# Optimization experiments

Hardware: AMD Instinct MI355X
Metric: run time of the kernel (lower is better)

## Reference

```python
import jax, jax.numpy as jnp
import numpy as np

WINDOW = 11
K1, K2, L, EPS = 0.01, 0.03, 1.0, 1e-8


def _box_filter(x, window):
    # Depthwise normalized box filter, VALID padding. x: (B, C, H, W)
    c = x.shape[1]
    k = jnp.ones((c, 1, window, window), dtype=x.dtype) / (window * window)
    return jax.lax.conv_general_dilated(
        x, k, window_strides=(1, 1), padding='VALID',
        dimension_numbers=('NCHW', 'OIHW', 'NCHW'),
        feature_group_count=c)


def setup_inputs() -> dict:
    key = jax.random.key(0)
    kx, ky = jax.random.split(key)
    shape = (16, 3, 512, 512)
    x = jax.random.uniform(kx, shape, dtype=jnp.float32)
    y = jax.random.uniform(ky, shape, dtype=jnp.float32)
    return {"x": x, "y": y}


def reference(x, y):
    C1 = (K1 * L) ** 2
    C2 = (K2 * L) ** 2
    mu_x = _box_filter(x, WINDOW)
    mu_y = _box_filter(y, WINDOW)
    mu_x_sq = mu_x * mu_x
    mu_y_sq = mu_y * mu_y
    mu_xy = mu_x * mu_y
    sigma_x_sq = jnp.maximum(_box_filter(x * x, WINDOW) - mu_x_sq, 0.0)
    sigma_y_sq = jnp.maximum(_box_filter(y * y, WINDOW) - mu_y_sq, 0.0)
    sigma_xy = _box_filter(x * y, WINDOW) - mu_xy
    num = (2.0 * mu_xy + C1) * (2.0 * sigma_xy + C2)
    den = (mu_x_sq + mu_y_sq + C1) * (sigma_x_sq + sigma_y_sq + C2) + EPS
    ssim = jnp.mean(num / den)
    return 1.0 - ssim
```

## Files before the change

### kernel.cpp

```cpp
#include <hip/hip_runtime.h>


#define WIN     11
#define IMG     512
#define OUTW    502
#define SEG     32
#define NSEG    16
#define NPLANES 48
#define RINGN   12
#define STRIDE  516

#define C1f     (0.01f * 0.01f)
#define C2f     (0.03f * 0.03f)
#define EPSf    1e-8f
#define INV121  (1.0f / 121.0f)

__global__ __launch_bounds__(128) void ssim_init(double* acc) {
    acc[0] = 0.0;
}

__global__ __launch_bounds__(128) void ssim_main(const float* __restrict__ x,
                                                 const float* __restrict__ y,
                                                 double* __restrict__ acc) {
    __shared__ float ring[2][RINGN][STRIDE];
    __shared__ float wsum[2];

    const int t     = threadIdx.x;
    const int plane = blockIdx.y;
    const int seg   = blockIdx.x;
    const int o0    = seg * SEG;
    const int o1    = (o0 + SEG < OUTW) ? (o0 + SEG) : OUTW;
    const int r0    = o0;
    const int r1    = o1 + WIN - 2;

    const float* xp = x + (size_t)plane * IMG * IMG;
    const float* yp = y + (size_t)plane * IMG * IMG;

    const int  c0     = 4 * t;
    const bool active = (c0 < OUTW);

    float Vx[14], Vy[14], Vxx[14], Vyy[14], Vxy[14];
#pragma unroll
    for (int j = 0; j < 14; ++j) { Vx[j]=0.f; Vy[j]=0.f; Vxx[j]=0.f; Vyy[j]=0.f; Vxy[j]=0.f; }

    float lsum = 0.0f;

    float4 px = ((const float4*)(xp + (size_t)r0 * IMG))[t];
    float4 py = ((const float4*)(yp + (size_t)r0 * IMG))[t];

    int slot = 0;
    for (int r = r0; r <= r1; ++r) {
        ((float4*)&ring[0][slot][0])[t] = px;
        ((float4*)&ring[1][slot][0])[t] = py;
        if (t < 4) { ring[0][slot][512 + t] = 0.0f; ring[1][slot][512 + t] = 0.0f; }
        if (r < r1) {
            px = ((const float4*)(xp + (size_t)(r + 1) * IMG))[t];
            py = ((const float4*)(yp + (size_t)(r + 1) * IMG))[t];
        }
        __syncthreads();

        if (active) {
            if (r - r0 >= WIN) {
                int os = slot - WIN; if (os < 0) os += RINGN;
                const float4* xr = (const float4*)&ring[0][os][0];
                const float4* yr = (const float4*)&ring[1][os][0];
                float4 a0 = xr[t], a1 = xr[t+1], a2 = xr[t+2], a3 = xr[t+3];
                float4 b0 = yr[t], b1 = yr[t+1], b2 = yr[t+2], b3 = yr[t+3];
                float xn[16], yn[16];
                xn[0]=a0.x; xn[1]=a0.y; xn[2]=a0.z; xn[3]=a0.w;
                xn[4]=a1.x; xn[5]=a1.y; xn[6]=a1.z; xn[7]=a1.w;
                xn[8]=a2.x; xn[9]=a2.y; xn[10]=a2.z; xn[11]=a2.w;
                xn[12]=a3.x; xn[13]=a3.y; xn[14]=a3.z; xn[15]=a3.w;
                yn[0]=b0.x; yn[1]=b0.y; yn[2]=b0.z; yn[3]=b0.w;
                yn[4]=b1.x; yn[5]=b1.y; yn[6]=b1.z; yn[7]=b1.w;
                yn[8]=b2.x; yn[9]=b2.y; yn[10]=b2.z; yn[11]=b2.w;
                yn[12]=b3.x; yn[13]=b3.y; yn[14]=b3.z; yn[15]=b3.w;
#pragma unroll
                for (int j = 0; j < 14; ++j) {
                    float xv = xn[j], yv = yn[j];
                    Vx[j]  -= xv;      Vy[j]  -= yv;
                    Vxx[j] -= xv * xv; Vyy[j] -= yv * yv; Vxy[j] -= xv * yv;
                }
            }
            {
                const float4* xr = (const float4*)&ring[0][slot][0];
                const float4* yr = (const float4*)&ring[1][slot][0];
                float4 a0 = xr[t], a1 = xr[t+1], a2 = xr[t+2], a3 = xr[t+3];
                float4 b0 = yr[t], b1 = yr[t+1], b2 = yr[t+2], b3 = yr[t+3];
                float xn[16], yn[16];
                xn[0]=a0.x; xn[1]=a0.y; xn[2]=a0.z; xn[3]=a0.w;
                xn[4]=a1.x; xn[5]=a1.y; xn[6]=a1.z; xn[7]=a1.w;
                xn[8]=a2.x; xn[9]=a2.y; xn[10]=a2.z; xn[11]=a2.w;
                xn[12]=a3.x; xn[13]=a3.y; xn[14]=a3.z; xn[15]=a3.w;
                yn[0]=b0.x; yn[1]=b0.y; yn[2]=b0.z; yn[3]=b0.w;
                yn[4]=b1.x; yn[5]=b1.y; yn[6]=b1.z; yn[7]=b1.w;
                yn[8]=b2.x; yn[9]=b2.y; yn[10]=b2.z; yn[11]=b2.w;
                yn[12]=b3.x; yn[13]=b3.y; yn[14]=b3.z; yn[15]=b3.w;
#pragma unroll
                for (int j = 0; j < 14; ++j) {
                    float xv = xn[j], yv = yn[j];
                    Vx[j]  += xv;      Vy[j]  += yv;
                    Vxx[j] += xv * xv; Vyy[j] += yv * yv; Vxy[j] += xv * yv;
                }
            }
            if (r - r0 >= WIN - 1) {
                float hx = 0.f, hy = 0.f, hxx = 0.f, hyy = 0.f, hxy = 0.f;
#pragma unroll
                for (int k = 0; k < WIN; ++k) {
                    hx += Vx[k]; hy += Vy[k]; hxx += Vxx[k]; hyy += Vyy[k]; hxy += Vxy[k];
                }
#pragma unroll
                for (int j = 0; j < 4; ++j) {
                    if (j > 0) {
                        hx  += Vx[j + 10]  - Vx[j - 1];
                        hy  += Vy[j + 10]  - Vy[j - 1];
                        hxx += Vxx[j + 10] - Vxx[j - 1];
                        hyy += Vyy[j + 10] - Vyy[j - 1];
                        hxy += Vxy[j + 10] - Vxy[j - 1];
                    }
                    if (c0 + j < OUTW) {
                        float mux = hx * INV121, muy = hy * INV121;
                        float ex2 = hxx * INV121, ey2 = hyy * INV121, exy = hxy * INV121;
                        float mxs = mux * mux, mys = muy * muy, mxy = mux * muy;
                        float sx  = fmaxf(ex2 - mxs, 0.0f);
                        float sy  = fmaxf(ey2 - mys, 0.0f);
                        float sxy = exy - mxy;
                        float num = (2.0f * mxy + C1f) * (2.0f * sxy + C2f);
                        float den = (mxs + mys + C1f) * (sx + sy + C2f) + EPSf;
                        lsum += num / den;
                    }
                }
            }
        }
        __syncthreads();
        if (++slot == RINGN) slot = 0;
    }

#pragma unroll
    for (int off = 32; off > 0; off >>= 1) lsum += __shfl_down(lsum, off, 64);
    const int wid = t >> 6, lane = t & 63;
    if (lane == 0) wsum[wid] = lsum;
    __syncthreads();
    if (t == 0) atomicAdd(acc, (double)(wsum[0] + wsum[1]));
}

__global__ __launch_bounds__(128) void ssim_final(const double* __restrict__ acc,
                                                  float* __restrict__ out) {
    const double N = (double)NPLANES * OUTW * OUTW;
    out[0] = 1.0f - (float)(acc[0] / N);
}

extern "C" void kernel_launch(void* const* d_in, const int* in_sizes, int n_in,
                              void* d_out, int out_size, void* d_ws, size_t ws_size,
                              hipStream_t stream) {
    const float* x = (const float*)d_in[0];
    const float* y = (const float*)d_in[1];
    float* out = (float*)d_out;
    double* acc = (double*)d_ws;

    ssim_init<<<dim3(1), dim3(128), 0, stream>>>(acc);
    ssim_main<<<dim3(NSEG, NPLANES), dim3(128), 0, stream>>>(x, y, acc);
    ssim_final<<<dim3(1), dim3(128), 0, stream>>>(acc, out);
}
```

Before: 149.1 us.

## Restructure SSIM: register vertical sums, shared horizontal pass, partial-sum reduction

Vertical running sums now live per thread in registers for its own 4 columns, with old rows re-read from global memory instead of a shared-memory ring. Only the vertical sums are written to double-buffered shared memory, and the horizontal 11-wide window is built from neighbouring float4s, which removes the 14-wide register arrays and one barrier per row. Segments are halved to launch more blocks. Per-block partial sums are written to workspace and reduced in a final kernel instead of using a global atomic plus an init kernel, and the divide is replaced by rcp with one Newton step. The cost is extra global traffic for the re-read rows and more halo overhead from shorter segments.

```diff
diff --git a/kernel.cpp b/kernel.cpp
--- a/kernel.cpp
+++ b/kernel.cpp
@@ -4,25 +4,26 @@
 #define WIN     11
 #define IMG     512
 #define OUTW    502
-#define SEG     32
-#define NSEG    16
+#define SEG     16
+#define NSEG    32
 #define NPLANES 48
-#define RINGN   12
-#define STRIDE  516
+#define NPART   (NSEG * NPLANES)
+#define HSTR    516
 
 #define C1f     (0.01f * 0.01f)
 #define C2f     (0.03f * 0.03f)
 #define EPSf    1e-8f
 #define INV121  (1.0f / 121.0f)
 
-__global__ __launch_bounds__(128) void ssim_init(double* acc) {
-    acc[0] = 0.0;
+__global__ __launch_bounds__(64) void ssim_zero(double* acc) {
+    if (threadIdx.x == 0) acc[0] = 0.0;
 }
 
 __global__ __launch_bounds__(128) void ssim_main(const float* __restrict__ x,
                                                  const float* __restrict__ y,
-                                                 double* __restrict__ acc) {
-    __shared__ float ring[2][RINGN][STRIDE];
+                                                 double* __restrict__ part,
+                                                 int mode) {
+    __shared__ float H[2][5][HSTR];
     __shared__ float wsum[2];
 
     const int t     = threadIdx.x;
@@ -33,107 +34,117 @@
     const int r0    = o0;
     const int r1    = o1 + WIN - 2;
 
-    const float* xp = x + (size_t)plane * IMG * IMG;
-    const float* yp = y + (size_t)plane * IMG * IMG;
+    const float4* xp4 = (const float4*)(x + (size_t)plane * IMG * IMG);
+    const float4* yp4 = (const float4*)(y + (size_t)plane * IMG * IMG);
 
     const int  c0     = 4 * t;
     const bool active = (c0 < OUTW);
 
-    float Vx[14], Vy[14], Vxx[14], Vyy[14], Vxy[14];
+    if (t < 4) {
 #pragma unroll
-    for (int j = 0; j < 14; ++j) { Vx[j]=0.f; Vy[j]=0.f; Vxx[j]=0.f; Vyy[j]=0.f; Vxy[j]=0.f; }
+        for (int b = 0; b < 2; ++b)
+#pragma unroll
+            for (int q = 0; q < 5; ++q)
+                H[b][q][512 + t] = 0.0f;
+    }
+
+    float Vx[4]  = {0.f, 0.f, 0.f, 0.f};
+    float Vy[4]  = {0.f, 0.f, 0.f, 0.f};
+    float Vxx[4] = {0.f, 0.f, 0.f, 0.f};
+    float Vyy[4] = {0.f, 0.f, 0.f, 0.f};
+    float Vxy[4] = {0.f, 0.f, 0.f, 0.f};
+
+    float4 nx = xp4[r0 * 128 + t];
+    float4 ny = yp4[r0 * 128 + t];
+    float4 ox = make_float4(0.f, 0.f, 0.f, 0.f);
+    float4 oy = make_float4(0.f, 0.f, 0.f, 0.f);
 
     float lsum = 0.0f;
+    int buf = 0;
 
-    float4 px = ((const float4*)(xp + (size_t)r0 * IMG))[t];
-    float4 py = ((const float4*)(yp + (size_t)r0 * IMG))[t];
+    for (int r = r0; r <= r1; ++r) {
+        float4 nx2 = nx, ny2 = ny, ox2 = ox, oy2 = oy;
+        if (r < r1) {
+            nx2 = xp4[(r + 1) * 128 + t];
+            ny2 = yp4[(r + 1) * 128 + t];
+            if (r - r0 >= WIN - 1) {
+                ox2 = xp4[(r + 1 - WIN) * 128 + t];
+                oy2 = yp4[(r + 1 - WIN) * 128 + t];
+            }
+        }
 
-    int slot = 0;
-    for (int r = r0; r <= r1; ++r) {
-        ((float4*)&ring[0][slot][0])[t] = px;
-        ((float4*)&ring[1][slot][0])[t] = py;
-        if (t < 4) { ring[0][slot][512 + t] = 0.0f; ring[1][slot][512 + t] = 0.0f; }
-        if (r < r1) {
-            px = ((const float4*)(xp + (size_t)(r + 1) * IMG))[t];
-            py = ((const float4*)(yp + (size_t)(r + 1) * IMG))[t];
+        if (r - r0 >= WIN) {
+            const float xo[4] = {ox.x, ox.y, ox.z, ox.w};
+            const float yo[4] = {oy.x, oy.y, oy.z, oy.w};
+#pragma unroll
+            for (int j = 0; j < 4; ++j) {
+                Vx[j] -= xo[j];
+                Vy[j] -= yo[j];
+                Vxx[j] = fmaf(-xo[j], xo[j], Vxx[j]);
+                Vyy[j] = fmaf(-yo[j], yo[j], Vyy[j]);
+                Vxy[j] = fmaf(-xo[j], yo[j], Vxy[j]);
+            }
         }
+        {
+            const float xn[4] = {nx.x, nx.y, nx.z, nx.w};
+            const float yn[4] = {ny.x, ny.y, ny.z, ny.w};
+#pragma unroll
+            for (int j = 0; j < 4; ++j) {
+                Vx[j] += xn[j];
+                Vy[j] += yn[j];
+                Vxx[j] = fmaf(xn[j], xn[j], Vxx[j]);
+                Vyy[j] = fmaf(yn[j], yn[j], Vyy[j]);
+                Vxy[j] = fmaf(xn[j], yn[j], Vxy[j]);
+            }
+        }
+
+        ((float4*)&H[buf][0][0])[t] = make_float4(Vx[0],  Vx[1],  Vx[2],  Vx[3]);
+        ((float4*)&H[buf][1][0])[t] = make_float4(Vy[0],  Vy[1],  Vy[2],  Vy[3]);
+        ((float4*)&H[buf][2][0])[t] = make_float4(Vxx[0], Vxx[1], Vxx[2], Vxx[3]);
+        ((float4*)&H[buf][3][0])[t] = make_float4(Vyy[0], Vyy[1], Vyy[2], Vyy[3]);
+        ((float4*)&H[buf][4][0])[t] = make_float4(Vxy[0], Vxy[1], Vxy[2], Vxy[3]);
         __syncthreads();
 
-        if (active) {
-            if (r - r0 >= WIN) {
-                int os = slot - WIN; if (os < 0) os += RINGN;
-                const float4* xr = (const float4*)&ring[0][os][0];
-                const float4* yr = (const float4*)&ring[1][os][0];
-                float4 a0 = xr[t], a1 = xr[t+1], a2 = xr[t+2], a3 = xr[t+3];
-                float4 b0 = yr[t], b1 = yr[t+1], b2 = yr[t+2], b3 = yr[t+3];
-                float xn[16], yn[16];
-                xn[0]=a0.x; xn[1]=a0.y; xn[2]=a0.z; xn[3]=a0.w;
-                xn[4]=a1.x; xn[5]=a1.y; xn[6]=a1.z; xn[7]=a1.w;
-                xn[8]=a2.x; xn[9]=a2.y; xn[10]=a2.z; xn[11]=a2.w;
-                xn[12]=a3.x; xn[13]=a3.y; xn[14]=a3.z; xn[15]=a3.w;
-                yn[0]=b0.x; yn[1]=b0.y; yn[2]=b0.z; yn[3]=b0.w;
-                yn[4]=b1.x; yn[5]=b1.y; yn[6]=b1.z; yn[7]=b1.w;
-                yn[8]=b2.x; yn[9]=b2.y; yn[10]=b2.z; yn[11]=b2.w;
-                yn[12]=b3.x; yn[13]=b3.y; yn[14]=b3.z; yn[15]=b3.w;
+        if (active && r - r0 >= WIN - 1) {
+            float hx[4], hy[4], hxx[4], hyy[4], hxy[4];
+#define HORIZ(V, q, h)                                                        \
+            {                                                                 \
+                const float4* rp = (const float4*)&H[buf][q][0];              \
+                float4 n1 = rp[t + 1], n2 = rp[t + 2], n3 = rp[t + 3];        \
+                h[0] = ((V[0] + V[1]) + (V[2] + V[3]))                        \
+                     + ((n1.x + n1.y) + (n1.z + n1.w))                        \
+                     + ((n2.x + n2.y) + n2.z);                                \
+                h[1] = h[0] - V[0] + n2.w;                                    \
+                h[2] = h[1] - V[1] + n3.x;                                    \
+                h[3] = h[2] - V[2] + n3.y;                                    \
+            }
+            HORIZ(Vx,  0, hx)
+            HORIZ(Vy,  1, hy)
+            HORIZ(Vxx, 2, hxx)
+            HORIZ(Vyy, 3, hyy)
+            HORIZ(Vxy, 4, hxy)
+#undef HORIZ
 #pragma unroll
-                for (int j = 0; j < 14; ++j) {
-                    float xv = xn[j], yv = yn[j];
-                    Vx[j]  -= xv;      Vy[j]  -= yv;
-                    Vxx[j] -= xv * xv; Vyy[j] -= yv * yv; Vxy[j] -= xv * yv;
-                }
-            }
-            {
-                const float4* xr = (const float4*)&ring[0][slot][0];
-                const float4* yr = (const float4*)&ring[1][slot][0];
-                float4 a0 = xr[t], a1 = xr[t+1], a2 = xr[t+2], a3 = xr[t+3];
-                float4 b0 = yr[t], b1 = yr[t+1], b2 = yr[t+2], b3 = yr[t+3];
-                float xn[16], yn[16];
-                xn[0]=a0.x; xn[1]=a0.y; xn[2]=a0.z; xn[3]=a0.w;
-                xn[4]=a1.x; xn[5]=a1.y; xn[6]=a1.z; xn[7]=a1.w;
-                xn[8]=a2.x; xn[9]=a2.y; xn[10]=a2.z; xn[11]=a2.w;
-                xn[12]=a3.x; xn[13]=a3.y; xn[14]=a3.z; xn[15]=a3.w;
-                yn[0]=b0.x; yn[1]=b0.y; yn[2]=b0.z; yn[3]=b0.w;
-                yn[4]=b1.x; yn[5]=b1.y; yn[6]=b1.z; yn[7]=b1.w;
-                yn[8]=b2.x; yn[9]=b2.y; yn[10]=b2.z; yn[11]=b2.w;
-                yn[12]=b3.x; yn[13]=b3.y; yn[14]=b3.z; yn[15]=b3.w;
-#pragma unroll
-                for (int j = 0; j < 14; ++j) {
-                    float xv = xn[j], yv = yn[j];
-                    Vx[j]  += xv;      Vy[j]  += yv;
-                    Vxx[j] += xv * xv; Vyy[j] += yv * yv; Vxy[j] += xv * yv;
-                }
-            }
-            if (r - r0 >= WIN - 1) {
-                float hx = 0.f, hy = 0.f, hxx = 0.f, hyy = 0.f, hxy = 0.f;
-#pragma unroll
-                for (int k = 0; k < WIN; ++k) {
-                    hx += Vx[k]; hy += Vy[k]; hxx += Vxx[k]; hyy += Vyy[k]; hxy += Vxy[k];
-                }
-#pragma unroll
-                for (int j = 0; j < 4; ++j) {
-                    if (j > 0) {
-                        hx  += Vx[j + 10]  - Vx[j - 1];
-                        hy  += Vy[j + 10]  - Vy[j - 1];
-                        hxx += Vxx[j + 10] - Vxx[j - 1];
-                        hyy += Vyy[j + 10] - Vyy[j - 1];
-                        hxy += Vxy[j + 10] - Vxy[j - 1];
-                    }
-                    if (c0 + j < OUTW) {
-                        float mux = hx * INV121, muy = hy * INV121;
-                        float ex2 = hxx * INV121, ey2 = hyy * INV121, exy = hxy * INV121;
-                        float mxs = mux * mux, mys = muy * muy, mxy = mux * muy;
-                        float sx  = fmaxf(ex2 - mxs, 0.0f);
-                        float sy  = fmaxf(ey2 - mys, 0.0f);
-                        float sxy = exy - mxy;
-                        float num = (2.0f * mxy + C1f) * (2.0f * sxy + C2f);
-                        float den = (mxs + mys + C1f) * (sx + sy + C2f) + EPSf;
-                        lsum += num / den;
-                    }
+            for (int j = 0; j < 4; ++j) {
+                if (c0 + j < OUTW) {
+                    float mux = hx[j]  * INV121, muy = hy[j]  * INV121;
+                    float ex2 = hxx[j] * INV121, ey2 = hyy[j] * INV121;
+                    float exy = hxy[j] * INV121;
+                    float mxs = mux * mux, mys = muy * muy, mxy = mux * muy;
+                    float sx  = fmaxf(fmaf(-mux, mux, ex2), 0.0f);
+                    float sy  = fmaxf(fmaf(-muy, muy, ey2), 0.0f);
+                    float sxy = exy - mxy;
+                    float num = fmaf(2.0f, mxy, C1f) * fmaf(2.0f, sxy, C2f);
+                    float den = fmaf(mxs + mys + C1f, sx + sy + C2f, EPSf);
+                    float rr  = __builtin_amdgcn_rcpf(den);
+                    rr = rr * (2.0f - den * rr);
+                    lsum = fmaf(num, rr, lsum);
                 }
             }
         }
-        __syncthreads();
-        if (++slot == RINGN) slot = 0;
+
+        buf ^= 1;
+        nx = nx2; ny = ny2; ox = ox2; oy = oy2;
     }
 
 #pragma unroll
@@ -141,13 +152,27 @@
     const int wid = t >> 6, lane = t & 63;
     if (lane == 0) wsum[wid] = lsum;
     __syncthreads();
-    if (t == 0) atomicAdd(acc, (double)(wsum[0] + wsum[1]));
+    if (t == 0) {
+        double bs = (double)(wsum[0] + wsum[1]);
+        if (mode == 0) part[blockIdx.y * NSEG + blockIdx.x] = bs;
+        else           atomicAdd(part, bs);
+    }
 }
 
-__global__ __launch_bounds__(128) void ssim_final(const double* __restrict__ acc,
-                                                  float* __restrict__ out) {
-    const double N = (double)NPLANES * OUTW * OUTW;
-    out[0] = 1.0f - (float)(acc[0] / N);
+__global__ __launch_bounds__(256) void ssim_final(const double* __restrict__ part,
+                                                  int n, float* __restrict__ out) {
+    __shared__ double s[4];
+    double v = 0.0;
+    for (int i = threadIdx.x; i < n; i += 256) v += part[i];
+#pragma unroll
+    for (int off = 32; off > 0; off >>= 1) v += __shfl_down(v, off, 64);
+    if ((threadIdx.x & 63) == 0) s[threadIdx.x >> 6] = v;
+    __syncthreads();
+    if (threadIdx.x == 0) {
+        double tot = s[0] + s[1] + s[2] + s[3];
+        const double N = (double)NPLANES * OUTW * OUTW;
+        out[0] = 1.0f - (float)(tot / N);
+    }
 }
 
 extern "C" void kernel_launch(void* const* d_in, const int* in_sizes, int n_in,
@@ -156,9 +181,14 @@
     const float* x = (const float*)d_in[0];
     const float* y = (const float*)d_in[1];
     float* out = (float*)d_out;
-    double* acc = (double*)d_ws;
+    double* part = (double*)d_ws;
 
-    ssim_init<<<dim3(1), dim3(128), 0, stream>>>(acc);
-    ssim_main<<<dim3(NSEG, NPLANES), dim3(128), 0, stream>>>(x, y, acc);
-    ssim_final<<<dim3(1), dim3(128), 0, stream>>>(acc, out);
+    if (ws_size >= (size_t)NPART * sizeof(double)) {
+        ssim_main<<<dim3(NSEG, NPLANES), dim3(128), 0, stream>>>(x, y, part, 0);
+        ssim_final<<<dim3(1), dim3(256), 0, stream>>>(part, NPART, out);
+    } else {
+        ssim_zero<<<dim3(1), dim3(64), 0, stream>>>(part);
+        ssim_main<<<dim3(NSEG, NPLANES), dim3(128), 0, stream>>>(x, y, part, 1);
+        ssim_final<<<dim3(1), dim3(256), 0, stream>>>(part, 1, out);
+    }
 }
```

New measurement: 140.4 us. 1.06x faster.
